# Performance work log

Hardware: AMD Instinct MI355X
Metric: run time of the kernel (lower is better)

## Reference

```python
import jax, jax.numpy as jnp
import numpy as np

TEMPERATURE = 0.07  # config['hyperparameter']['temperature']
EPS = 1e-12         # F.normalize default eps


def _l2norm(x):
    return x / jnp.maximum(jnp.linalg.norm(x, axis=-1, keepdims=True), EPS)


def _forward(labels, features, prototypes, num_class):
    # forward_base of Prototype_Balanced_Contrastive_Loss (step == 0 path).
    B, C, H, W = features.shape
    K = num_class + 1          # classes 0..num_class (0 = background, excluded)
    Pn = H * W
    lab = labels.reshape(B, Pn)               # labels already at feature res -> nearest interp is identity
    feats = features.reshape(B, C, Pn)

    # per-(batch, class) masked mean over pixels (vectorized segmented reduction)
    onehot = (lab[:, :, None] == jnp.arange(K)[None, None, :]).astype(features.dtype)  # [B,P,K]
    counts = onehot.sum(axis=1)                                  # [B,K]
    sums = jnp.einsum('bcp,bpk->bkc', feats, onehot)             # [B,K,C]
    means = sums / jnp.maximum(counts, 1.0)[..., None]
    proto_b = _l2norm(means)                                     # [B,K,C]

    cls_ids = jnp.arange(K)
    present = (counts > 0) & (cls_ids[None, :] >= 1)             # class 0 skipped, 255 out of range

    # global prototype (detached) appended as last slot for every class >= 1
    g = _l2norm(jax.lax.stop_gradient(prototypes))               # [K,C]
    batch_slots = jnp.where(present.T[:, :, None], jnp.swapaxes(proto_b, 0, 1), 0.0)   # [K,B,C]
    glob_slot = jnp.where((cls_ids >= 1)[:, None, None], g[:, None, :], 0.0)           # [K,1,C]
    protos = jnp.concatenate([batch_slots, glob_slot], axis=1)   # [K,B+1,C]
    valid = jnp.concatenate([present.T, (cls_ids >= 1)[:, None]], axis=1)              # [K,B+1]
    cnt = valid.sum(axis=1).astype(features.dtype)               # cnt_class

    # all-pairs similarities between prototype slots
    S = jnp.einsum('ksc,mnc->ksmn', protos, protos) / TEMPERATURE        # [K,B+1,K,B+1]
    E = jnp.exp(S) * valid[None, None, :, :].astype(features.dtype)
    # denominator: sum_m (1/cnt_m) sum_n exp(sim)  (class 0 masked out by valid)
    den = (E.sum(axis=3) / jnp.maximum(cnt, 1.0)[None, None, :]).sum(axis=2)           # [K,B+1]

    # positive logits: same-class slots, excluding self (k != j)
    S_same = jnp.moveaxis(jnp.diagonal(S, axis1=0, axis2=2), -1, 0)      # [K,B+1,B+1]
    diag = jnp.diagonal(S_same, axis1=1, axis2=2)                        # [K,B+1]
    pos_sum = (S_same * valid[:, None, :].astype(features.dtype)).sum(axis=2) - diag

    n_pos = cnt[:, None] - 1.0                                           # number of k != j terms
    # anchors: batch-slot prototypes only (j ranges over first cnt-1 slots = batch protos)
    anchor_mask = (valid & (jnp.arange(B + 1) < B)[None, :]).astype(features.dtype)
    # sum_k -log(exp(s_k)/den) / (cnt-1)^2 = -(pos_sum - n_pos*log(den)) / (cnt-1)^2
    per_anchor = -(pos_sum - n_pos * jnp.log(den)) / jnp.maximum(n_pos, 1.0) ** 2
    total = (per_anchor * anchor_mask).sum()

    cnt_exist = ((cnt > 1.0) & (cls_ids >= 1)).sum().astype(features.dtype)
    return 0.1 * total / cnt_exist


def setup_inputs() -> dict:
    key = jax.random.key(0)
    kl, kf, kp = jax.random.split(key, 3)
    B, C, H, W, NC = 16, 256, 128, 128, 100
    return {
        "labels": jax.random.randint(kl, (B, H, W), 0, NC + 1),
        "features": jax.random.normal(kf, (B, C, H, W), dtype=jnp.float32),
        "prototypes": jax.random.normal(kp, (NC + 1, C), dtype=jnp.float32),
        "num_class": NC,
    }


def reference(labels, features, prototypes, num_class):
    return _forward(labels, features, prototypes, num_class)
```

## Files before the change

### kernel.cpp

```cpp
#include <hip/hip_runtime.h>
#include <hip/hip_bf16.h>
#include <math.h>

#define B_    16
#define C_    256
#define P_    16384
#define K_    101
#define S_    17
#define V_    1717
#define GN_   1792
#define NPQ_  4
#define TEMP_ 0.07f
#define INV_SQRT_T 3.7796447300922720f

typedef __bf16 bf16x8 __attribute__((ext_vector_type(8)));
typedef float f32x4 __attribute__((ext_vector_type(4)));
typedef int   i32x4 __attribute__((ext_vector_type(4)));

__device__ __forceinline__ void atomAddGlb(float* p, float v) {
  __hip_atomic_fetch_add(p, v, __ATOMIC_RELAXED, __HIP_MEMORY_SCOPE_AGENT);
}

__device__ __forceinline__ unsigned packHiLo(float x) {
  const unsigned u = __float_as_uint(x);
  const unsigned h = u & 0xFFFF0000u;
  const unsigned l = __float_as_uint(x - __uint_as_float(h));
  return __builtin_amdgcn_perm(l, u, 0x07060302u);
}

__global__ __launch_bounds__(512, 4) void k_segsum(
    const int* __restrict__ labels, const float* __restrict__ feats,
    float* __restrict__ psum, unsigned* __restrict__ counts) {
  __shared__ unsigned s_cnt[102];
  __shared__ f32x4 s_red[2][512];
  const int id = blockIdx.x;
  const int tid = threadIdx.x;

  if (id >= 512) {
    const int b = id - 512;
    if (tid < 102) s_cnt[tid] = 0u;
    __syncthreads();
    for (int i = 0; i < 32; ++i) {
      int lab = labels[b * P_ + i * 512 + tid];
      if ((unsigned)lab > 100u) lab = 101;
      atomicAdd(&s_cnt[lab], 1u);
    }
    __syncthreads();
    if (tid < K_) counts[b * K_ + tid] = s_cnt[tid];
    return;
  }

  const int cg = id & 7, pqg = (id >> 3) & 3, b = id >> 5;
  const int wv = tid >> 6, ln = tid & 63;
  const int lg = ln >> 4;
  const int lc = ln & 15;
  const int pq = pqg * 8 + wv;
  const int pbase = pq * 512;
  const int* lptr = labels + b * P_ + pbase + lg * 4;
  const float* fbase =
      feats + ((size_t)b * C_ + cg * 32 + lc) * P_ + pbase + lg * 4;

  f32x4 acc[2][7];
#pragma unroll
  for (int ct = 0; ct < 2; ++ct)
#pragma unroll
    for (int t = 0; t < 7; ++t) acc[ct][t] = (f32x4)0.f;

  for (int w = 0; w < 16; ++w) {
    const int off = w * 32;
    const i32x4 la0 = *(const i32x4*)&lptr[off];
    const i32x4 la1 = *(const i32x4*)&lptr[off + 16];
    int d0[4], d1[4];
#pragma unroll
    for (int r = 0; r < 4; ++r) { d0[r] = la0[r] - lc; d1[r] = la1[r] - lc; }
    i32x4 p0[2], p1[2];
#pragma unroll
    for (int ct = 0; ct < 2; ++ct) {
      const float4 f0 = *(const float4*)&fbase[(size_t)ct * 16 * P_ + off];
      const float4 f1 = *(const float4*)&fbase[(size_t)ct * 16 * P_ + off + 16];
      p0[ct][0] = (int)packHiLo(f0.x); p0[ct][1] = (int)packHiLo(f0.y);
      p0[ct][2] = (int)packHiLo(f0.z); p0[ct][3] = (int)packHiLo(f0.w);
      p1[ct][0] = (int)packHiLo(f1.x); p1[ct][1] = (int)packHiLo(f1.y);
      p1[ct][2] = (int)packHiLo(f1.z); p1[ct][3] = (int)packHiLo(f1.w);
    }
    const bf16x8 b00 = __builtin_bit_cast(bf16x8, p0[0]);
    const bf16x8 b10 = __builtin_bit_cast(bf16x8, p1[0]);
    const bf16x8 b01 = __builtin_bit_cast(bf16x8, p0[1]);
    const bf16x8 b11 = __builtin_bit_cast(bf16x8, p1[1]);
#pragma unroll
    for (int t = 0; t < 7; ++t) {
      const int m0 = t * 16;
      i32x4 a0v, a1v;
#pragma unroll
      for (int r = 0; r < 4; ++r) {
        a0v[r] = (d0[r] == m0) ? (int)0x3F803F80 : 0;
        a1v[r] = (d1[r] == m0) ? (int)0x3F803F80 : 0;
      }
      const bf16x8 a0 = __builtin_bit_cast(bf16x8, a0v);
      const bf16x8 a1 = __builtin_bit_cast(bf16x8, a1v);
      acc[0][t] = __builtin_amdgcn_mfma_f32_16x16x32_bf16(a0, b00, acc[0][t], 0, 0, 0);
      acc[0][t] = __builtin_amdgcn_mfma_f32_16x16x32_bf16(a1, b10, acc[0][t], 0, 0, 0);
      acc[1][t] = __builtin_amdgcn_mfma_f32_16x16x32_bf16(a0, b01, acc[1][t], 0, 0, 0);
      acc[1][t] = __builtin_amdgcn_mfma_f32_16x16x32_bf16(a1, b11, acc[1][t], 0, 0, 0);
    }
  }
  float* pbas = psum + ((size_t)(pqg * 16 + b) * K_) * 256 + cg * 32;
#pragma unroll
  for (int t = 0; t < 7; ++t) {
    s_red[0][wv * 64 + ln] = acc[0][t];
    s_red[1][wv * 64 + ln] = acc[1][t];
    __syncthreads();
    if (wv < 2) {
      f32x4 s = (f32x4)0.f;
#pragma unroll
      for (int g = 0; g < 8; ++g) {
        const f32x4 v = s_red[wv][g * 64 + ln];
        s[0] += v[0]; s[1] += v[1]; s[2] += v[2]; s[3] += v[3];
      }
#pragma unroll
      for (int r = 0; r < 4; ++r) {
        const int row = t * 16 + lg * 4 + r;
        if (row < K_)
          pbas[(size_t)row * 256 + wv * 16 + lc] = s[r];
      }
    }
    __syncthreads();
  }
}

__global__ __launch_bounds__(512) void k_protos(
    const float* __restrict__ psum, const unsigned* __restrict__ counts,
    const float* __restrict__ prototypes, unsigned short* __restrict__ PmH,
    unsigned short* __restrict__ PmL, float* __restrict__ wcol,
    float* __restrict__ cntk, float* __restrict__ scal) {
  const int k = blockIdx.x;
  const int tid = threadIdx.x, wv = tid >> 6, ln = tid & 63;
  __shared__ int s_valid[S_];
  for (int s = wv; s < S_; s += 8) {
    float val[4];
    int pres;
    if (s < B_) {
      const unsigned cb = counts[s * K_ + k];
      float4 v = {0.f, 0.f, 0.f, 0.f};
#pragma unroll
      for (int pq = 0; pq < NPQ_; ++pq) {
        const float4 t4 =
            *(const float4*)&psum[((size_t)(pq * 16 + s) * K_ + k) * 256 + ln * 4];
        v.x += t4.x; v.y += t4.y; v.z += t4.z; v.w += t4.w;
      }
      const float cbf = fmaxf((float)cb, 1.f);
      val[0] = v.x / cbf; val[1] = v.y / cbf; val[2] = v.z / cbf; val[3] = v.w / cbf;
      pres = (cb > 0u) && (k >= 1);
    } else {
      const float4 pv4 = *(const float4*)&prototypes[k * C_ + ln * 4];
      val[0] = pv4.x; val[1] = pv4.y; val[2] = pv4.z; val[3] = pv4.w;
      pres = (k >= 1);
    }
    float ss = val[0] * val[0] + val[1] * val[1] + val[2] * val[2] + val[3] * val[3];
#pragma unroll
    for (int m = 1; m < 64; m <<= 1) ss += __shfl_xor(ss, m);
    const float nrm = fmaxf(sqrtf(ss), 1e-12f);
    unsigned short h[4], l[4];
#pragma unroll
    for (int j = 0; j < 4; ++j) {
      const float pv = pres ? (val[j] / nrm) * INV_SQRT_T : 0.f;
      const unsigned u = __float_as_uint(pv);
      const float lo = pv - __uint_as_float(u & 0xFFFF0000u);
      h[j] = (unsigned short)(u >> 16);
      l[j] = (unsigned short)(__float_as_uint(lo) >> 16);
    }
    const size_t idx = ((size_t)k * S_ + s) * C_ + ln * 4;
    *(ushort4*)&PmH[idx] = make_ushort4(h[0], h[1], h[2], h[3]);
    *(ushort4*)&PmL[idx] = make_ushort4(l[0], l[1], l[2], l[3]);
    if (ln == 0) s_valid[s] = pres;
  }
  __syncthreads();
  if (tid == 0) {
    int cnt = 0;
    for (int s = 0; s < S_; ++s) cnt += s_valid[s];
    const float cf = (float)cnt;
    cntk[k] = cf;
    const float wvv = 1.f / fmaxf(cf, 1.f);
    for (int s = 0; s < S_; ++s)
      wcol[k * S_ + s] = s_valid[s] ? wvv : 0.f;
    if (cnt > 1 && k >= 1) atomAddGlb(&scal[1], 1.f);
  }
}

__global__ __launch_bounds__(256) void k_gramloss(
    const unsigned short* __restrict__ PmH,
    const unsigned short* __restrict__ PmL, const float* __restrict__ wcol,
    float* __restrict__ den, float* __restrict__ pos) {
  const int tid = threadIdx.x;
  const int wv = tid >> 6, ln = tid & 63;
  const int gid = blockIdx.x * 4 + wv;
  const int ri = gid / 28, cj = gid % 28;
  const int lg = ln >> 4, lc = ln & 15;

  f32x4 acc[4][4];
#pragma unroll
  for (int m = 0; m < 4; ++m)
#pragma unroll
    for (int n = 0; n < 4; ++n) acc[m][n] = (f32x4)0.f;

#pragma unroll
  for (int ks = 0; ks < 8; ++ks) {
    const int kb = ks * 32 + lg * 8;
    bf16x8 aH[4], aL[4], bH[4], bL[4];
#pragma unroll
    for (int m = 0; m < 4; ++m) {
      const size_t ra = (size_t)(ri * 64 + m * 16 + lc) * C_ + kb;
      aH[m] = __builtin_bit_cast(bf16x8, *(const i32x4*)&PmH[ra]);
      aL[m] = __builtin_bit_cast(bf16x8, *(const i32x4*)&PmL[ra]);
      const size_t rb = (size_t)(cj * 64 + m * 16 + lc) * C_ + kb;
      bH[m] = __builtin_bit_cast(bf16x8, *(const i32x4*)&PmH[rb]);
      bL[m] = __builtin_bit_cast(bf16x8, *(const i32x4*)&PmL[rb]);
    }
#pragma unroll
    for (int m = 0; m < 4; ++m)
#pragma unroll
      for (int n = 0; n < 4; ++n) {
        acc[m][n] = __builtin_amdgcn_mfma_f32_16x16x32_bf16(aH[m], bH[n], acc[m][n], 0, 0, 0);
        acc[m][n] = __builtin_amdgcn_mfma_f32_16x16x32_bf16(aH[m], bL[n], acc[m][n], 0, 0, 0);
        acc[m][n] = __builtin_amdgcn_mfma_f32_16x16x32_bf16(aL[m], bH[n], acc[m][n], 0, 0, 0);
      }
  }
  float wc[4];
  int cabs[4], ccls[4];
#pragma unroll
  for (int n = 0; n < 4; ++n) {
    cabs[n] = cj * 64 + n * 16 + lc;
    wc[n] = (cabs[n] < V_) ? wcol[cabs[n]] : 0.f;
    ccls[n] = cabs[n] / S_;
  }
  f32x4 denP[4], posP[4];
#pragma unroll
  for (int m = 0; m < 4; ++m) {
    denP[m] = (f32x4)0.f;
    posP[m] = (f32x4)0.f;
    const int rbase = ri * 64 + m * 16 + lg * 4;
#pragma unroll
    for (int r = 0; r < 4; ++r) {
      const int rabs = rbase + r;
      const int rcls = rabs / S_;
#pragma unroll
      for (int n = 0; n < 4; ++n) {
        const float g = acc[m][n][r];
        denP[m][r] += wc[n] * __expf(g);
        if (ccls[n] == rcls && wc[n] > 0.f && cabs[n] != rabs)
          posP[m][r] += g;
      }
    }
  }
#pragma unroll
  for (int msk = 1; msk <= 8; msk <<= 1)
#pragma unroll
    for (int m = 0; m < 4; ++m)
#pragma unroll
      for (int r = 0; r < 4; ++r) {
        denP[m][r] += __shfl_xor(denP[m][r], msk);
        posP[m][r] += __shfl_xor(posP[m][r], msk);
      }
  if (lc == 0) {
#pragma unroll
    for (int m = 0; m < 4; ++m)
#pragma unroll
      for (int r = 0; r < 4; ++r) {
        const int rabs = ri * 64 + m * 16 + lg * 4 + r;
        if (rabs < V_) {
          atomAddGlb(&den[rabs], denP[m][r]);
          atomAddGlb(&pos[rabs], posP[m][r]);
        }
      }
  }
}

__global__ __launch_bounds__(1024) void k_final(
    const float* __restrict__ den, const float* __restrict__ pos,
    const float* __restrict__ wcol, const float* __restrict__ cntk,
    const float* __restrict__ scal, float* __restrict__ out) {
  const int tid = threadIdx.x;
  float tot = 0.f;
  for (int a = tid; a < V_; a += 1024) {
    const int k = a / S_, s = a - k * S_;
    if (s >= B_ || k < 1 || wcol[a] <= 0.f) continue;
    const float np = cntk[k] - 1.f;
    const float npc = fmaxf(np, 1.f);
    tot += -(pos[a] - np * logf(den[a])) / (npc * npc);
  }
#pragma unroll
  for (int m = 1; m < 64; m <<= 1) tot += __shfl_xor(tot, m);
  __shared__ float red[16];
  if ((tid & 63) == 0) red[tid >> 6] = tot;
  __syncthreads();
  if (tid == 0) {
    float t = 0.f;
#pragma unroll
    for (int i = 0; i < 16; ++i) t += red[i];
    out[0] = 0.1f * t / scal[1];
  }
}

extern "C" void kernel_launch(void* const* d_in, const int* in_sizes, int n_in,
                              void* d_out, int out_size, void* d_ws, size_t ws_size,
                              hipStream_t stream) {
  const int* labels = (const int*)d_in[0];
  const float* feats = (const float*)d_in[1];
  const float* protos = (const float*)d_in[2];
  float* out = (float*)d_out;

  char* wsb = (char*)d_ws;
  size_t o = 0;
  auto nxt = [&](size_t bytes) {
    size_t r = o;
    o = (o + bytes + 255) & ~(size_t)255;
    return r;
  };
  const size_t off_cnts = nxt((size_t)B_ * K_ * 4);
  const size_t off_PH   = nxt((size_t)GN_ * C_ * 2);
  const size_t off_PL   = nxt((size_t)GN_ * C_ * 2);
  const size_t off_w    = nxt((size_t)GN_ * 4);
  const size_t off_cntk = nxt((size_t)K_ * 4);
  const size_t off_scal = nxt(8);
  const size_t off_den  = nxt((size_t)V_ * 4);
  const size_t off_pos  = nxt((size_t)V_ * 4);
  const size_t small_end = o;
  const size_t off_psum = nxt((size_t)NPQ_ * 16 * K_ * 256 * 4);
  (void)off_psum;

  unsigned* w_cnts = (unsigned*)(wsb + off_cnts);
  unsigned short* w_PH = (unsigned short*)(wsb + off_PH);
  unsigned short* w_PL = (unsigned short*)(wsb + off_PL);
  float* w_w       = (float*)(wsb + off_w);
  float* w_cntk    = (float*)(wsb + off_cntk);
  float* w_scal    = (float*)(wsb + off_scal);
  float* w_den     = (float*)(wsb + off_den);
  float* w_pos     = (float*)(wsb + off_pos);
  float* w_psum    = (float*)(wsb + off_psum);

  hipMemsetAsync(d_ws, 0, small_end, stream);

  k_segsum<<<528, 512, 0, stream>>>(labels, feats, w_psum, w_cnts);
  k_protos<<<K_, 512, 0, stream>>>(w_psum, w_cnts, protos, w_PH, w_PL,
                                   w_w, w_cntk, w_scal);
  k_gramloss<<<196, 256, 0, stream>>>(w_PH, w_PL, w_w, w_den, w_pos);
  k_final<<<1, 1024, 0, stream>>>(w_den, w_pos, w_w, w_cntk, w_scal, out);
}
```

Before: 87.38 us.

## Restructure segmented-sum kernel to full-pixel blocks and drop partial-sum pass

The segmented reduction now gives each 1024-thread block all pixels of one batch for a 16-channel slice, instead of splitting pixels into four partial-sum groups. Partial sums no longer go to a scratch buffer that k_protos must add up, and the block's cross-wave reduction is done in a single shared-memory pass. In exchange each wave handles one 16-channel tile rather than two, so the label loads and one-hot construction are reused across half as many MFMAs. The grid also shrinks to 272 larger blocks using more shared memory, which may lower occupancy and latency hiding in this memory-bound pass.

```diff
diff --git a/kernel.cpp b/kernel.cpp
--- a/kernel.cpp
+++ b/kernel.cpp
@@ -9,7 +9,6 @@
 #define S_    17
 #define V_    1717
 #define GN_   1792
-#define NPQ_  4
 #define TEMP_ 0.07f
 #define INV_SQRT_T 3.7796447300922720f
 
@@ -28,20 +27,20 @@
   return __builtin_amdgcn_perm(l, u, 0x07060302u);
 }
 
-__global__ __launch_bounds__(512, 4) void k_segsum(
+__global__ __launch_bounds__(1024, 4) void k_segsum(
     const int* __restrict__ labels, const float* __restrict__ feats,
-    float* __restrict__ psum, unsigned* __restrict__ counts) {
+    float* __restrict__ sums, unsigned* __restrict__ counts) {
+  __shared__ __align__(16) f32x4 s_red[7 * 16 * 64];
   __shared__ unsigned s_cnt[102];
-  __shared__ f32x4 s_red[2][512];
   const int id = blockIdx.x;
   const int tid = threadIdx.x;
 
-  if (id >= 512) {
-    const int b = id - 512;
+  if (id >= 256) {
+    const int b = id - 256;
     if (tid < 102) s_cnt[tid] = 0u;
     __syncthreads();
-    for (int i = 0; i < 32; ++i) {
-      int lab = labels[b * P_ + i * 512 + tid];
+    for (int i = 0; i < 16; ++i) {
+      int lab = labels[b * P_ + i * 1024 + tid];
       if ((unsigned)lab > 100u) lab = 101;
       atomicAdd(&s_cnt[lab], 1u);
     }
@@ -50,43 +49,35 @@
     return;
   }
 
-  const int cg = id & 7, pqg = (id >> 3) & 3, b = id >> 5;
+  const int cg = id & 15, b = id >> 4;
   const int wv = tid >> 6, ln = tid & 63;
   const int lg = ln >> 4;
   const int lc = ln & 15;
-  const int pq = pqg * 8 + wv;
-  const int pbase = pq * 512;
+  const int pbase = wv * 1024;
   const int* lptr = labels + b * P_ + pbase + lg * 4;
-  const float* fbase =
-      feats + ((size_t)b * C_ + cg * 32 + lc) * P_ + pbase + lg * 4;
-
-  f32x4 acc[2][7];
-#pragma unroll
-  for (int ct = 0; ct < 2; ++ct)
-#pragma unroll
-    for (int t = 0; t < 7; ++t) acc[ct][t] = (f32x4)0.f;
-
-  for (int w = 0; w < 16; ++w) {
+  const float* frow =
+      feats + ((size_t)b * C_ + cg * 16 + lc) * P_ + pbase + lg * 4;
+
+  f32x4 acc[7];
+#pragma unroll
+  for (int t = 0; t < 7; ++t) acc[t] = (f32x4)0.f;
+
+  for (int w = 0; w < 32; ++w) {
     const int off = w * 32;
     const i32x4 la0 = *(const i32x4*)&lptr[off];
     const i32x4 la1 = *(const i32x4*)&lptr[off + 16];
+    const float4 f0 = *(const float4*)&frow[off];
+    const float4 f1 = *(const float4*)&frow[off + 16];
+    i32x4 p0, p1;
+    p0[0] = (int)packHiLo(f0.x); p0[1] = (int)packHiLo(f0.y);
+    p0[2] = (int)packHiLo(f0.z); p0[3] = (int)packHiLo(f0.w);
+    p1[0] = (int)packHiLo(f1.x); p1[1] = (int)packHiLo(f1.y);
+    p1[2] = (int)packHiLo(f1.z); p1[3] = (int)packHiLo(f1.w);
+    const bf16x8 b0 = __builtin_bit_cast(bf16x8, p0);
+    const bf16x8 b1 = __builtin_bit_cast(bf16x8, p1);
     int d0[4], d1[4];
 #pragma unroll
     for (int r = 0; r < 4; ++r) { d0[r] = la0[r] - lc; d1[r] = la1[r] - lc; }
-    i32x4 p0[2], p1[2];
-#pragma unroll
-    for (int ct = 0; ct < 2; ++ct) {
-      const float4 f0 = *(const float4*)&fbase[(size_t)ct * 16 * P_ + off];
-      const float4 f1 = *(const float4*)&fbase[(size_t)ct * 16 * P_ + off + 16];
-      p0[ct][0] = (int)packHiLo(f0.x); p0[ct][1] = (int)packHiLo(f0.y);
-      p0[ct][2] = (int)packHiLo(f0.z); p0[ct][3] = (int)packHiLo(f0.w);
-      p1[ct][0] = (int)packHiLo(f1.x); p1[ct][1] = (int)packHiLo(f1.y);
-      p1[ct][2] = (int)packHiLo(f1.z); p1[ct][3] = (int)packHiLo(f1.w);
-    }
-    const bf16x8 b00 = __builtin_bit_cast(bf16x8, p0[0]);
-    const bf16x8 b10 = __builtin_bit_cast(bf16x8, p1[0]);
-    const bf16x8 b01 = __builtin_bit_cast(bf16x8, p0[1]);
-    const bf16x8 b11 = __builtin_bit_cast(bf16x8, p1[1]);
 #pragma unroll
     for (int t = 0; t < 7; ++t) {
       const int m0 = t * 16;
@@ -96,40 +87,34 @@
         a0v[r] = (d0[r] == m0) ? (int)0x3F803F80 : 0;
         a1v[r] = (d1[r] == m0) ? (int)0x3F803F80 : 0;
       }
-      const bf16x8 a0 = __builtin_bit_cast(bf16x8, a0v);
-      const bf16x8 a1 = __builtin_bit_cast(bf16x8, a1v);
-      acc[0][t] = __builtin_amdgcn_mfma_f32_16x16x32_bf16(a0, b00, acc[0][t], 0, 0, 0);
-      acc[0][t] = __builtin_amdgcn_mfma_f32_16x16x32_bf16(a1, b10, acc[0][t], 0, 0, 0);
-      acc[1][t] = __builtin_amdgcn_mfma_f32_16x16x32_bf16(a0, b01, acc[1][t], 0, 0, 0);
-      acc[1][t] = __builtin_amdgcn_mfma_f32_16x16x32_bf16(a1, b11, acc[1][t], 0, 0, 0);
-    }
-  }
-  float* pbas = psum + ((size_t)(pqg * 16 + b) * K_) * 256 + cg * 32;
-#pragma unroll
-  for (int t = 0; t < 7; ++t) {
-    s_red[0][wv * 64 + ln] = acc[0][t];
-    s_red[1][wv * 64 + ln] = acc[1][t];
-    __syncthreads();
-    if (wv < 2) {
-      f32x4 s = (f32x4)0.f;
-#pragma unroll
-      for (int g = 0; g < 8; ++g) {
-        const f32x4 v = s_red[wv][g * 64 + ln];
-        s[0] += v[0]; s[1] += v[1]; s[2] += v[2]; s[3] += v[3];
-      }
-#pragma unroll
-      for (int r = 0; r < 4; ++r) {
-        const int row = t * 16 + lg * 4 + r;
-        if (row < K_)
-          pbas[(size_t)row * 256 + wv * 16 + lc] = s[r];
-      }
-    }
-    __syncthreads();
+      acc[t] = __builtin_amdgcn_mfma_f32_16x16x32_bf16(
+          __builtin_bit_cast(bf16x8, a0v), b0, acc[t], 0, 0, 0);
+      acc[t] = __builtin_amdgcn_mfma_f32_16x16x32_bf16(
+          __builtin_bit_cast(bf16x8, a1v), b1, acc[t], 0, 0, 0);
+    }
+  }
+#pragma unroll
+  for (int t = 0; t < 7; ++t) s_red[(t * 16 + wv) * 64 + ln] = acc[t];
+  __syncthreads();
+  if (wv < 7) {
+    const int t = wv;
+    f32x4 s = (f32x4)0.f;
+#pragma unroll
+    for (int g = 0; g < 16; ++g) {
+      const f32x4 v = s_red[(t * 16 + g) * 64 + ln];
+      s[0] += v[0]; s[1] += v[1]; s[2] += v[2]; s[3] += v[3];
+    }
+    float* pbas = sums + (size_t)b * K_ * 256 + cg * 16 + lc;
+#pragma unroll
+    for (int r = 0; r < 4; ++r) {
+      const int row = t * 16 + lg * 4 + r;
+      if (row < K_) pbas[(size_t)row * 256] = s[r];
+    }
   }
 }
 
 __global__ __launch_bounds__(512) void k_protos(
-    const float* __restrict__ psum, const unsigned* __restrict__ counts,
+    const float* __restrict__ sums, const unsigned* __restrict__ counts,
     const float* __restrict__ prototypes, unsigned short* __restrict__ PmH,
     unsigned short* __restrict__ PmL, float* __restrict__ wcol,
     float* __restrict__ cntk, float* __restrict__ scal) {
@@ -141,13 +126,8 @@
     int pres;
     if (s < B_) {
       const unsigned cb = counts[s * K_ + k];
-      float4 v = {0.f, 0.f, 0.f, 0.f};
-#pragma unroll
-      for (int pq = 0; pq < NPQ_; ++pq) {
-        const float4 t4 =
-            *(const float4*)&psum[((size_t)(pq * 16 + s) * K_ + k) * 256 + ln * 4];
-        v.x += t4.x; v.y += t4.y; v.z += t4.z; v.w += t4.w;
-      }
+      const float4 v =
+          *(const float4*)&sums[((size_t)s * K_ + k) * 256 + ln * 4];
       const float cbf = fmaxf((float)cb, 1.f);
       val[0] = v.x / cbf; val[1] = v.y / cbf; val[2] = v.z / cbf; val[3] = v.w / cbf;
       pres = (cb > 0u) && (k >= 1);
@@ -316,7 +296,6 @@
     o = (o + bytes + 255) & ~(size_t)255;
     return r;
   };
-  const size_t off_cnts = nxt((size_t)B_ * K_ * 4);
   const size_t off_PH   = nxt((size_t)GN_ * C_ * 2);
   const size_t off_PL   = nxt((size_t)GN_ * C_ * 2);
   const size_t off_w    = nxt((size_t)GN_ * 4);
@@ -325,10 +304,9 @@
   const size_t off_den  = nxt((size_t)V_ * 4);
   const size_t off_pos  = nxt((size_t)V_ * 4);
   const size_t small_end = o;
-  const size_t off_psum = nxt((size_t)NPQ_ * 16 * K_ * 256 * 4);
-  (void)off_psum;
-
-  unsigned* w_cnts = (unsigned*)(wsb + off_cnts);
+  const size_t off_cnts = nxt((size_t)B_ * K_ * 4);
+  const size_t off_sums = nxt((size_t)B_ * K_ * 256 * 4);
+
   unsigned short* w_PH = (unsigned short*)(wsb + off_PH);
   unsigned short* w_PL = (unsigned short*)(wsb + off_PL);
   float* w_w       = (float*)(wsb + off_w);
@@ -336,12 +314,13 @@
   float* w_scal    = (float*)(wsb + off_scal);
   float* w_den     = (float*)(wsb + off_den);
   float* w_pos     = (float*)(wsb + off_pos);
-  float* w_psum    = (float*)(wsb + off_psum);
+  unsigned* w_cnts = (unsigned*)(wsb + off_cnts);
+  float* w_sums    = (float*)(wsb + off_sums);
 
   hipMemsetAsync(d_ws, 0, small_end, stream);
 
-  k_segsum<<<528, 512, 0, stream>>>(labels, feats, w_psum, w_cnts);
-  k_protos<<<K_, 512, 0, stream>>>(w_psum, w_cnts, protos, w_PH, w_PL,
+  k_segsum<<<272, 1024, 0, stream>>>(labels, feats, w_sums, w_cnts);
+  k_protos<<<K_, 512, 0, stream>>>(w_sums, w_cnts, protos, w_PH, w_PL,
                                    w_w, w_cntk, w_scal);
   k_gramloss<<<196, 256, 0, stream>>>(w_PH, w_PL, w_w, w_den, w_pos);
   k_final<<<1, 1024, 0, stream>>>(w_den, w_pos, w_w, w_cntk, w_scal, out);
```

Measured after the change: 92.77 us. 6.2% more time.
